# Kernel optimization log

Hardware: AMD Instinct MI355X
Metric: run time of the kernel (lower is better)

## Reference

```python
import jax, jax.numpy as jnp
import numpy as np

N_HEADS = 16
EPS = 1e-12  # F.normalize default eps


def setup_inputs() -> dict:
    key = jax.random.key(0)
    ks = jax.random.split(key, 12)
    bs, qlen, dim = 2, 2048, 2048
    s = 0.02
    return {
        "input": jax.random.normal(ks[0], (bs, qlen, dim), jnp.float32),
        "mask": jax.random.randint(ks[1], (bs, qlen), 0, 2, jnp.int64),
        "Wq": jax.random.normal(ks[2], (dim, dim), jnp.float32) * s,
        "bq": jax.random.normal(ks[3], (dim,), jnp.float32) * s,
        "Wk": jax.random.normal(ks[4], (dim, dim), jnp.float32) * s,
        "bk": jax.random.normal(ks[5], (dim,), jnp.float32) * s,
        "Wv": jax.random.normal(ks[6], (dim, dim), jnp.float32) * s,
        "bv": jax.random.normal(ks[7], (dim,), jnp.float32) * s,
        "Wo": jax.random.normal(ks[8], (dim, dim), jnp.float32) * s,
        "bo": jax.random.normal(ks[9], (dim,), jnp.float32) * s,
        "attention_scale": jnp.asarray(1.0 / np.sqrt(dim // N_HEADS), jnp.float32),
    }


def _l2norm(x):
    n = jnp.sqrt(jnp.sum(x * x, axis=-1, keepdims=True))
    return x / jnp.maximum(n, EPS)


def reference(input, mask, Wq, bq, Wk, bk, Wv, bv, Wo, bo, attention_scale):
    bs, qlen, dim = input.shape
    dph = dim // N_HEADS

    def shape(x):  # [b, s, dim] -> [b, h, s, dph]
        return x.reshape(bs, -1, N_HEADS, dph).transpose(0, 2, 1, 3)

    q = shape(input @ Wq.T + bq)
    k = shape(input @ Wk.T + bk)
    v = shape(input @ Wv.T + bv)

    # normalized (cosine) attention with learned scale
    q = _l2norm(q) * attention_scale
    k = _l2norm(k)

    scores = jnp.einsum("bhqd,bhkd->bhqk", q, k)
    masked = (mask == 0)[:, None, None, :]  # [b,1,1,klen]
    scores = jnp.where(masked, -jnp.inf, scores)
    weights = jax.nn.softmax(scores.astype(jnp.float32), axis=-1).astype(scores.dtype)
    # dropout p=0.0 / eval mode -> identity
    context = jnp.einsum("bhqk,bhkd->bhqd", weights, v)
    context = context.transpose(0, 2, 1, 3).reshape(bs, qlen, dim)
    return context @ Wo.T + bo
```

## Files before the change

### kernel.cpp

```cpp
#include <hip/hip_runtime.h>
#include <hip/hip_bf16.h>
#include <stdint.h>


typedef __attribute__((ext_vector_type(8))) short bf16x8;
typedef __attribute__((ext_vector_type(4))) float f32x4;
typedef __attribute__((ext_vector_type(8))) unsigned short u16x8;

#define XN 8388608L
#define WN 4194304L

__device__ __forceinline__ float bf2f(unsigned short u) {
  union { unsigned int i; float f; } v; v.i = ((unsigned int)u) << 16; return v.f;
}
__device__ __forceinline__ unsigned short f2bf(float f) {
  union { float f; unsigned int i; } u; u.f = f;
  unsigned int r = u.i + 0x7FFFu + ((u.i >> 16) & 1u);
  return (unsigned short)(r >> 16);
}

__device__ __forceinline__ void gload_lds16(const void* g, void* l) {
  __builtin_amdgcn_global_load_lds((__attribute__((address_space(1))) void*)g,
                                   (__attribute__((address_space(3))) void*)l,
                                   16, 0, 0);
}

__global__ __launch_bounds__(256) void cast5_kernel(
    const float* __restrict__ x,  const float* __restrict__ w0,
    const float* __restrict__ w1, const float* __restrict__ w2,
    const float* __restrict__ w3, unsigned short* __restrict__ dst,
    const int* __restrict__ mask, float* __restrict__ biasf)
{
  const long total8 = (XN + 4 * WN) >> 3;
  const long tid0 = (long)blockIdx.x * blockDim.x + threadIdx.x;
  const long stride = (long)gridDim.x * blockDim.x;
  for (long i = tid0; i < total8; i += stride) {
    long e = i << 3;
    const float* src; long off;
    if (e < XN) { src = x; off = e; }
    else {
      long r = e - XN;
      int wi = (int)(r >> 22);
      off = r & (WN - 1);
      src = (wi == 0) ? w0 : (wi == 1) ? w1 : (wi == 2) ? w2 : w3;
    }
    const float4* p = (const float4*)(src + off);
    float4 a = p[0], b = p[1];
    u16x8 o;
    o[0] = f2bf(a.x); o[1] = f2bf(a.y); o[2] = f2bf(a.z); o[3] = f2bf(a.w);
    o[4] = f2bf(b.x); o[5] = f2bf(b.y); o[6] = f2bf(b.z); o[7] = f2bf(b.w);
    *(u16x8*)(dst + e) = o;
  }
  for (long j = tid0; j < 4096; j += stride)
    biasf[j] = (mask[j] != 0) ? 0.f : -1.0e5f;
}

template<int OUT_BF16>
__global__ __launch_bounds__(256) void gemm_bt(
    const unsigned short* __restrict__ A, const unsigned short* __restrict__ B,
    const float* __restrict__ bias, void* __restrict__ Cout,
    int M, int N, int K)
{
  __shared__ unsigned short As[128 * 32];
  __shared__ unsigned short Bs[128 * 32];
  const int t    = threadIdx.x;
  const int lane = t & 63;
  const int w    = t >> 6;
  const int wr   = w >> 1, wc = w & 1;
  const int l15  = lane & 15;
  const int koff = (lane >> 4) * 8;
  const int lg4  = (lane >> 4) * 4;

  const long Kl = K;
  const unsigned short* Ag0 = A + (long)(blockIdx.y * 128 + (t >> 2)) * Kl + (t & 3) * 8;
  const unsigned short* Bg0 = B + (long)(blockIdx.x * 128 + (t >> 2)) * Kl + (t & 3) * 8;
  unsigned short* Asl = As + t * 8;
  unsigned short* Bsl = Bs + t * 8;

  f32x4 acc[4][4];
  const f32x4 zero = {0.f, 0.f, 0.f, 0.f};
  #pragma unroll
  for (int m = 0; m < 4; m++)
    #pragma unroll
    for (int n = 0; n < 4; n++) acc[m][n] = zero;

  const int nK = K >> 5;
  for (int kk = 0; kk < nK; kk++) {
    const long ko = (long)kk * 32;
    gload_lds16(Ag0 + ko,            Asl);
    gload_lds16(Ag0 + 64 * Kl + ko,  Asl + 2048);
    gload_lds16(Bg0 + ko,            Bsl);
    gload_lds16(Bg0 + 64 * Kl + ko,  Bsl + 2048);
    __syncthreads();
    bf16x8 af[4], bfr[4];
    #pragma unroll
    for (int m = 0; m < 4; m++)
      af[m] = *(const bf16x8*)&As[(wr * 64 + m * 16 + l15) * 32 + koff];
    #pragma unroll
    for (int n = 0; n < 4; n++)
      bfr[n] = *(const bf16x8*)&Bs[(wc * 64 + n * 16 + l15) * 32 + koff];
    #pragma unroll
    for (int m = 0; m < 4; m++)
      #pragma unroll
      for (int n = 0; n < 4; n++)
        acc[m][n] = __builtin_amdgcn_mfma_f32_16x16x32_bf16(af[m], bfr[n], acc[m][n], 0, 0, 0);
    __syncthreads();
  }

  #pragma unroll
  for (int m = 0; m < 4; m++) {
    const int row = blockIdx.y * 128 + wr * 64 + m * 16 + lg4;
    #pragma unroll
    for (int n = 0; n < 4; n++) {
      const int col = blockIdx.x * 128 + wc * 64 + n * 16 + l15;
      const float bv = bias[col];
      #pragma unroll
      for (int r = 0; r < 4; r++) {
        float v = acc[m][n][r] + bv;
        if (OUT_BF16) ((unsigned short*)Cout)[(long)(row + r) * N + col] = f2bf(v);
        else          ((float*)Cout)[(long)(row + r) * N + col] = v;
      }
    }
  }
}

__global__ __launch_bounds__(256) void norm_qk(unsigned short* __restrict__ Q,
                                               unsigned short* __restrict__ Kb,
                                               const float* __restrict__ scale_p)
{
  const int w = threadIdx.x >> 6, lane = threadIdx.x & 63;
  const long id = (long)blockIdx.x * 4 + w;
  const int isK = id >= 65536;
  const long p = isK ? id - 65536 : id;
  unsigned short* base = (isK ? Kb : Q) + (p >> 4) * 2048 + (p & 15) * 128 + lane * 2;
  unsigned int v = *(const unsigned int*)base;
  float x0 = bf2f((unsigned short)(v & 0xffffu));
  float x1 = bf2f((unsigned short)(v >> 16));
  float ss = x0 * x0 + x1 * x1;
  ss += __shfl_xor(ss, 1);  ss += __shfl_xor(ss, 2);  ss += __shfl_xor(ss, 4);
  ss += __shfl_xor(ss, 8);  ss += __shfl_xor(ss, 16); ss += __shfl_xor(ss, 32);
  float inv = rsqrtf(fmaxf(ss, 1e-24f));
  if (!isK) inv *= *scale_p;
  unsigned int o = (unsigned int)f2bf(x0 * inv) | ((unsigned int)f2bf(x1 * inv) << 16);
  *(unsigned int*)base = o;
}

__global__ __launch_bounds__(256) void transpose_v(const unsigned short* __restrict__ V,
                                                   unsigned short* __restrict__ Vt)
{
  __shared__ unsigned short tile[64][66];
  const int bh = blockIdx.z;
  const int b = bh >> 4, h = bh & 15;
  const int s0 = blockIdx.x * 64;
  const int d0 = blockIdx.y * 64;
  const int t = threadIdx.x;
  const int c = t & 63, r4 = t >> 6;
  #pragma unroll
  for (int i = 0; i < 16; i++) {
    int r = r4 + i * 4;
    tile[r][c] = V[(long)(b * 2048 + s0 + r) * 2048 + h * 128 + d0 + c];
  }
  __syncthreads();
  #pragma unroll
  for (int i = 0; i < 16; i++) {
    int dd = r4 + i * 4;
    Vt[((long)bh * 128 + d0 + dd) * 2048 + s0 + c] = tile[c][dd];
  }
}

__global__ __launch_bounds__(256, 2) void attn_kernel(
    const unsigned short* __restrict__ Q,
    const unsigned short* __restrict__ Kg_,
    const unsigned short* __restrict__ Vt_,
    const float* __restrict__ biasArr,
    unsigned short* __restrict__ ctx)
{
  __shared__ unsigned char KS[16384];
  __shared__ unsigned char VS[16384];
  __shared__ unsigned short Pl[4][32][72];

  const int bh = blockIdx.y, b = bh >> 4, h = bh & 15;
  const int t = threadIdx.x, w = t >> 6, lane = t & 63;
  const int l15 = lane & 15, lg = lane >> 4;
  const int xork = (l15 & 7) << 4;
  const int qrow0 = blockIdx.x * 128 + w * 32;

  bf16x8 aq[2][4];
  #pragma unroll
  for (int m = 0; m < 2; m++)
    #pragma unroll
    for (int dk = 0; dk < 4; dk++)
      aq[m][dk] = *(const bf16x8*)&Q[(long)(b * 2048 + qrow0 + m * 16 + l15) * 2048
                                     + h * 128 + dk * 32 + lg * 8];

  const char* Kgp = (const char*)(Kg_ + (long)b * 2048 * 2048 + h * 128);
  const char* Vgp = (const char*)(Vt_ + (long)bh * 128 * 2048);
  const int rK = t >> 4;
  const int rV = t >> 3;
  const char* srcK0 = Kgp + (long)rK * 4096 + (((t & 15) * 16) ^ ((rK & 7) << 4));
  const char* srcV0 = Vgp + (long)rV * 4096 + (((t & 7) * 16) ^ ((rV & 7) << 4));
  char* dstK0 = (char*)KS + t * 16;
  char* dstV0 = (char*)VS + t * 16;

  f32x4 o[2][8]; float den[2][4];
  const f32x4 zero = {0.f, 0.f, 0.f, 0.f};
  #pragma unroll
  for (int m = 0; m < 2; m++) {
    #pragma unroll
    for (int df = 0; df < 8; df++) o[m][df] = zero;
    #pragma unroll
    for (int r = 0; r < 4; r++) den[m][r] = 0.f;
  }

  const char* KSc = (const char*)KS;
  const char* VSc = (const char*)VS;
  int cK[4], cV2[2];
  #pragma unroll
  for (int dk = 0; dk < 4; dk++) cK[dk] = (dk * 64 + lg * 16) ^ xork;
  #pragma unroll
  for (int kk = 0; kk < 2; kk++) cV2[kk] = (kk * 64 + lg * 16) ^ xork;
  const int rowK = l15 * 256, rowV = l15 * 128;

  #pragma unroll
  for (int i = 0; i < 4; i++) gload_lds16(srcK0 + i * 65536,  dstK0 + i * 4096);
  #pragma unroll
  for (int i = 0; i < 4; i++) gload_lds16(srcV0 + i * 131072, dstV0 + i * 4096);

  const float* brow = biasArr + b * 2048 + l15;
  const float L2E = 1.44269504088896f;

  for (int kt = 0; kt < 32; kt++) {
    const int k0 = kt * 64;
    asm volatile("s_waitcnt vmcnt(4)" ::: "memory");
    __builtin_amdgcn_s_barrier();
    __builtin_amdgcn_sched_barrier(0);

    float bn[4];
    #pragma unroll
    for (int n = 0; n < 4; n++) bn[n] = brow[k0 + n * 16];

    f32x4 s[2][4];
    #pragma unroll
    for (int m = 0; m < 2; m++)
      #pragma unroll
      for (int n = 0; n < 4; n++) s[m][n] = zero;
    __builtin_amdgcn_s_setprio(1);
    #pragma unroll
    for (int n = 0; n < 4; n++) {
      #pragma unroll
      for (int dk = 0; dk < 4; dk++) {
        bf16x8 bk = *(const bf16x8*)(KSc + n * 4096 + rowK + cK[dk]);
        s[0][n] = __builtin_amdgcn_mfma_f32_16x16x32_bf16(aq[0][dk], bk, s[0][n], 0, 0, 0);
        s[1][n] = __builtin_amdgcn_mfma_f32_16x16x32_bf16(aq[1][dk], bk, s[1][n], 0, 0, 0);
      }
    }
    __builtin_amdgcn_s_setprio(0);

    #pragma unroll
    for (int n = 0; n < 4; n++) {
      #pragma unroll
      for (int m = 0; m < 2; m++) {
        #pragma unroll
        for (int r = 0; r < 4; r++) {
          float e = exp2f(fmaf(s[m][n][r], L2E, bn[n]));
          den[m][r] += e;
          Pl[w][m * 16 + lg * 4 + r][n * 16 + l15] = f2bf(e);
        }
      }
    }

    asm volatile("s_waitcnt vmcnt(0)" ::: "memory");
    __builtin_amdgcn_s_barrier();
    __builtin_amdgcn_sched_barrier(0);
    if (kt < 31) {
      const long kof = (long)(kt + 1) * 262144;
      #pragma unroll
      for (int i = 0; i < 4; i++) gload_lds16(srcK0 + kof + i * 65536, dstK0 + i * 4096);
    }

    #pragma unroll
    for (int kk = 0; kk < 2; kk++) {
      bf16x8 ap0 = *(const bf16x8*)&Pl[w][l15][kk * 32 + lg * 8];
      bf16x8 ap1 = *(const bf16x8*)&Pl[w][16 + l15][kk * 32 + lg * 8];
      bf16x8 bv[8];
      #pragma unroll
      for (int df = 0; df < 8; df++)
        bv[df] = *(const bf16x8*)(VSc + df * 2048 + rowV + cV2[kk]);
      __builtin_amdgcn_s_setprio(1);
      #pragma unroll
      for (int df = 0; df < 8; df++) {
        o[0][df] = __builtin_amdgcn_mfma_f32_16x16x32_bf16(ap0, bv[df], o[0][df], 0, 0, 0);
        o[1][df] = __builtin_amdgcn_mfma_f32_16x16x32_bf16(ap1, bv[df], o[1][df], 0, 0, 0);
      }
      __builtin_amdgcn_s_setprio(0);
    }

    __builtin_amdgcn_s_barrier();
    __builtin_amdgcn_sched_barrier(0);
    if (kt < 31) {
      const long vof = (long)(kt + 1) * 128;
      #pragma unroll
      for (int i = 0; i < 4; i++) gload_lds16(srcV0 + vof + i * 131072, dstV0 + i * 4096);
    }
  }

  #pragma unroll
  for (int m = 0; m < 2; m++)
    #pragma unroll
    for (int r = 0; r < 4; r++) {
      float d = den[m][r];
      d += __shfl_xor(d, 1); d += __shfl_xor(d, 2);
      d += __shfl_xor(d, 4); d += __shfl_xor(d, 8);
      den[m][r] = 1.0f / d;
    }
  #pragma unroll
  for (int m = 0; m < 2; m++) {
    const long row = b * 2048 + qrow0 + m * 16 + lg * 4;
    #pragma unroll
    for (int df = 0; df < 8; df++) {
      const int col = h * 128 + df * 16 + l15;
      #pragma unroll
      for (int r = 0; r < 4; r++)
        ctx[(row + r) * 2048 + col] = f2bf(o[m][df][r] * den[m][r]);
    }
  }
}

extern "C" void kernel_launch(void* const* d_in, const int* in_sizes, int n_in,
                              void* d_out, int out_size, void* d_ws, size_t ws_size,
                              hipStream_t stream) {
  const float* x    = (const float*)d_in[0];
  const int*   mask = (const int*)d_in[1];
  const float* Wq   = (const float*)d_in[2];
  const float* bq   = (const float*)d_in[3];
  const float* Wk   = (const float*)d_in[4];
  const float* bk   = (const float*)d_in[5];
  const float* Wv   = (const float*)d_in[6];
  const float* bv   = (const float*)d_in[7];
  const float* Wo   = (const float*)d_in[8];
  const float* bo   = (const float*)d_in[9];
  const float* asc  = (const float*)d_in[10];
  float* out = (float*)d_out;

  unsigned short* w   = (unsigned short*)d_ws;
  unsigned short* Xb  = w;
  unsigned short* Wqb = Xb  + XN;
  unsigned short* Wkb = Wqb + WN;
  unsigned short* Wvb = Wkb + WN;
  unsigned short* Wob = Wvb + WN;
  unsigned short* Qb  = Wob + WN;
  unsigned short* Kbf = Qb  + XN;
  unsigned short* Vb  = Kbf + XN;
  unsigned short* Vt  = Vb  + XN;
  float*          Bias = (float*)(Vt + XN);
  unsigned short* Ctx = Xb;

  cast5_kernel<<<2048, 256, 0, stream>>>(x, Wq, Wk, Wv, Wo, Xb, mask, Bias);

  dim3 g(16, 32);
  gemm_bt<1><<<g, 256, 0, stream>>>(Xb, Wqb, bq, Qb,  4096, 2048, 2048);
  gemm_bt<1><<<g, 256, 0, stream>>>(Xb, Wkb, bk, Kbf, 4096, 2048, 2048);
  gemm_bt<1><<<g, 256, 0, stream>>>(Xb, Wvb, bv, Vb,  4096, 2048, 2048);

  norm_qk<<<32768, 256, 0, stream>>>(Qb, Kbf, asc);
  transpose_v<<<dim3(32, 2, 32), 256, 0, stream>>>(Vb, Vt);

  attn_kernel<<<dim3(16, 32), 256, 0, stream>>>(Qb, Kbf, Vt, Bias, Ctx);

  gemm_bt<0><<<g, 256, 0, stream>>>(Ctx, Wob, bo, out, 4096, 2048, 2048);
}
```

Baseline: 488.7 us.

## Double-buffer GEMM LDS, fuse Q/K projections, compute V transposed directly

Replaces the GEMM kernel with a double-buffered version that prefetches the next K-slice into LDS while MFMAs run, using raw barriers and setprio. Q and K projections now run in one launch, and tile IDs are remapped to group blocks across XCDs. V is computed as Wv·X^T so the GEMM writes V already transposed, which removes the separate transpose kernel and its extra memory round trip. The cost is double the LDS use and a hard-coded K=2048 and matrix sizes.

```diff
diff --git a/kernel.cpp b/kernel.cpp
--- a/kernel.cpp
+++ b/kernel.cpp
@@ -55,14 +55,27 @@
     biasf[j] = (mask[j] != 0) ? 0.f : -1.0e5f;
 }
 
-template<int OUT_BF16>
-__global__ __launch_bounds__(256) void gemm_bt(
-    const unsigned short* __restrict__ A, const unsigned short* __restrict__ B,
-    const float* __restrict__ bias, void* __restrict__ Cout,
-    int M, int N, int K)
+template<int MODE>
+__global__ __launch_bounds__(256) void gemm2(
+    const unsigned short* __restrict__ A, const unsigned short* __restrict__ Bmat,
+    const float* __restrict__ bias0, const float* __restrict__ bias1,
+    void* __restrict__ Cout)
 {
-  __shared__ unsigned short As[128 * 32];
-  __shared__ unsigned short Bs[128 * 32];
+  constexpr int NWG = (MODE == 0) ? 1024 : 512;
+  __shared__ unsigned short As[2][4096];
+  __shared__ unsigned short Bs[2][4096];
+
+  const int bid = blockIdx.x;
+  const int id = (bid & 7) * (NWG / 8) + (bid >> 3);
+
+  int mat, bx, by;
+  if (MODE == 0)      { mat = id >> 9; int rem = id & 511; bx = rem & 15; by = rem >> 4; }
+  else if (MODE == 1) { mat = 0; bx = id & 31; by = id >> 5; }
+  else                { mat = 0; bx = id & 15; by = id >> 4; }
+
+  const unsigned short* Bb = (MODE == 0) ? (Bmat + (long)mat * WN) : Bmat;
+  const float* bias = (MODE == 0) ? (mat ? bias1 : bias0) : bias0;
+
   const int t    = threadIdx.x;
   const int lane = t & 63;
   const int w    = t >> 6;
@@ -71,11 +84,8 @@
   const int koff = (lane >> 4) * 8;
   const int lg4  = (lane >> 4) * 4;
 
-  const long Kl = K;
-  const unsigned short* Ag0 = A + (long)(blockIdx.y * 128 + (t >> 2)) * Kl + (t & 3) * 8;
-  const unsigned short* Bg0 = B + (long)(blockIdx.x * 128 + (t >> 2)) * Kl + (t & 3) * 8;
-  unsigned short* Asl = As + t * 8;
-  unsigned short* Bsl = Bs + t * 8;
+  const unsigned short* Ag0 = A  + (long)(by * 128 + (t >> 2)) * 2048 + (t & 3) * 8;
+  const unsigned short* Bg0 = Bb + (long)(bx * 128 + (t >> 2)) * 2048 + (t & 3) * 8;
 
   f32x4 acc[4][4];
   const f32x4 zero = {0.f, 0.f, 0.f, 0.f};
@@ -84,41 +94,65 @@
     #pragma unroll
     for (int n = 0; n < 4; n++) acc[m][n] = zero;
 
-  const int nK = K >> 5;
-  for (int kk = 0; kk < nK; kk++) {
+  auto stage = [&](int buf, int kk) {
     const long ko = (long)kk * 32;
-    gload_lds16(Ag0 + ko,            Asl);
-    gload_lds16(Ag0 + 64 * Kl + ko,  Asl + 2048);
-    gload_lds16(Bg0 + ko,            Bsl);
-    gload_lds16(Bg0 + 64 * Kl + ko,  Bsl + 2048);
-    __syncthreads();
+    gload_lds16(Ag0 + ko,              &As[buf][t * 8]);
+    gload_lds16(Ag0 + 64 * 2048 + ko,  &As[buf][t * 8 + 2048]);
+    gload_lds16(Bg0 + ko,              &Bs[buf][t * 8]);
+    gload_lds16(Bg0 + 64 * 2048 + ko,  &Bs[buf][t * 8 + 2048]);
+  };
+
+  auto body = [&](int bufR, int kk, int bufW) {
+    if (kk + 1 < 64) stage(bufW, kk + 1);
     bf16x8 af[4], bfr[4];
     #pragma unroll
     for (int m = 0; m < 4; m++)
-      af[m] = *(const bf16x8*)&As[(wr * 64 + m * 16 + l15) * 32 + koff];
+      af[m] = *(const bf16x8*)&As[bufR][(wr * 64 + m * 16 + l15) * 32 + koff];
     #pragma unroll
     for (int n = 0; n < 4; n++)
-      bfr[n] = *(const bf16x8*)&Bs[(wc * 64 + n * 16 + l15) * 32 + koff];
+      bfr[n] = *(const bf16x8*)&Bs[bufR][(wc * 64 + n * 16 + l15) * 32 + koff];
+    __builtin_amdgcn_s_setprio(1);
     #pragma unroll
     for (int m = 0; m < 4; m++)
       #pragma unroll
       for (int n = 0; n < 4; n++)
         acc[m][n] = __builtin_amdgcn_mfma_f32_16x16x32_bf16(af[m], bfr[n], acc[m][n], 0, 0, 0);
-    __syncthreads();
+    __builtin_amdgcn_s_setprio(0);
+    asm volatile("s_waitcnt vmcnt(0)" ::: "memory");
+    __builtin_amdgcn_s_barrier();
+    __builtin_amdgcn_sched_barrier(0);
+  };
+
+  stage(0, 0);
+  asm volatile("s_waitcnt vmcnt(0)" ::: "memory");
+  __builtin_amdgcn_s_barrier();
+  __builtin_amdgcn_sched_barrier(0);
+
+  for (int kk = 0; kk < 64; kk += 2) {
+    body(0, kk,     1);
+    body(1, kk + 1, 0);
   }
 
   #pragma unroll
   for (int m = 0; m < 4; m++) {
-    const int row = blockIdx.y * 128 + wr * 64 + m * 16 + lg4;
+    const int row = by * 128 + wr * 64 + m * 16 + lg4;
     #pragma unroll
     for (int n = 0; n < 4; n++) {
-      const int col = blockIdx.x * 128 + wc * 64 + n * 16 + l15;
-      const float bv = bias[col];
+      const int col = bx * 128 + wc * 64 + n * 16 + l15;
       #pragma unroll
       for (int r = 0; r < 4; r++) {
-        float v = acc[m][n][r] + bv;
-        if (OUT_BF16) ((unsigned short*)Cout)[(long)(row + r) * N + col] = f2bf(v);
-        else          ((float*)Cout)[(long)(row + r) * N + col] = v;
+        float v = acc[m][n][r];
+        if (MODE == 0) {
+          v += bias[col];
+          ((unsigned short*)Cout + (long)mat * XN)[(long)(row + r) * 2048 + col] = f2bf(v);
+        } else if (MODE == 1) {
+          v += bias[row + r];
+          ((unsigned short*)Cout)[(long)(row + r) * 2048 + (col & 2047)
+                                  + (long)(col >> 11) * 4194304] = f2bf(v);
+        } else {
+          v += bias[col];
+          ((float*)Cout)[(long)(row + r) * 2048 + col] = v;
+        }
       }
     }
   }
@@ -145,29 +179,6 @@
   *(unsigned int*)base = o;
 }
 
-__global__ __launch_bounds__(256) void transpose_v(const unsigned short* __restrict__ V,
-                                                   unsigned short* __restrict__ Vt)
-{
-  __shared__ unsigned short tile[64][66];
-  const int bh = blockIdx.z;
-  const int b = bh >> 4, h = bh & 15;
-  const int s0 = blockIdx.x * 64;
-  const int d0 = blockIdx.y * 64;
-  const int t = threadIdx.x;
-  const int c = t & 63, r4 = t >> 6;
-  #pragma unroll
-  for (int i = 0; i < 16; i++) {
-    int r = r4 + i * 4;
-    tile[r][c] = V[(long)(b * 2048 + s0 + r) * 2048 + h * 128 + d0 + c];
-  }
-  __syncthreads();
-  #pragma unroll
-  for (int i = 0; i < 16; i++) {
-    int dd = r4 + i * 4;
-    Vt[((long)bh * 128 + d0 + dd) * 2048 + s0 + c] = tile[c][dd];
-  }
-}
-
 __global__ __launch_bounds__(256, 2) void attn_kernel(
     const unsigned short* __restrict__ Q,
     const unsigned short* __restrict__ Kg_,
@@ -345,27 +356,22 @@
   unsigned short* w   = (unsigned short*)d_ws;
   unsigned short* Xb  = w;
   unsigned short* Wqb = Xb  + XN;
-  unsigned short* Wkb = Wqb + WN;
-  unsigned short* Wvb = Wkb + WN;
+  unsigned short* Wvb = Wqb + 2 * WN;
   unsigned short* Wob = Wvb + WN;
   unsigned short* Qb  = Wob + WN;
   unsigned short* Kbf = Qb  + XN;
-  unsigned short* Vb  = Kbf + XN;
-  unsigned short* Vt  = Vb  + XN;
+  unsigned short* Vt  = Kbf + XN;
   float*          Bias = (float*)(Vt + XN);
   unsigned short* Ctx = Xb;
 
   cast5_kernel<<<2048, 256, 0, stream>>>(x, Wq, Wk, Wv, Wo, Xb, mask, Bias);
 
-  dim3 g(16, 32);
-  gemm_bt<1><<<g, 256, 0, stream>>>(Xb, Wqb, bq, Qb,  4096, 2048, 2048);
-  gemm_bt<1><<<g, 256, 0, stream>>>(Xb, Wkb, bk, Kbf, 4096, 2048, 2048);
-  gemm_bt<1><<<g, 256, 0, stream>>>(Xb, Wvb, bv, Vb,  4096, 2048, 2048);
+  gemm2<0><<<1024, 256, 0, stream>>>(Xb, Wqb, bq, bk, Qb);
+  gemm2<1><<<512,  256, 0, stream>>>(Wvb, Xb, bv, bv, Vt);
 
   norm_qk<<<32768, 256, 0, stream>>>(Qb, Kbf, asc);
-  transpose_v<<<dim3(32, 2, 32), 256, 0, stream>>>(Vb, Vt);
 
   attn_kernel<<<dim3(16, 32), 256, 0, stream>>>(Qb, Kbf, Vt, Bias, Ctx);
 
-  gemm_bt<0><<<g, 256, 0, stream>>>(Ctx, Wob, bo, out, 4096, 2048, 2048);
-}
+  gemm2<2><<<512, 256, 0, stream>>>(Ctx, Wob, bo, bo, out);
+}
```

Result: faster. 459.5 us (-6.0%).
